# Kernel tuning notes

Measured on AMD Instinct MI355X. Metric: run time of the kernel, lower is better.

## Reference

```python
import jax, jax.numpy as jnp
import numpy as np

N_ATOMS = 2048
REPLICATES = 3          # fixed in source
CENTER_CELL = 13        # index of (0,0,0) offset among the 27 images


def setup_inputs() -> dict:
    key = jax.random.key(0)
    k1, k2, k3 = jax.random.split(key, 3)
    # Slightly perturbed cubic lattice, ~30 Angstrom box
    cell = 30.0 * jnp.eye(3, dtype=jnp.float32) + 0.5 * jax.random.normal(k1, (3, 3), dtype=jnp.float32)
    frac = jax.random.uniform(k2, (N_ATOMS, 3), dtype=jnp.float32)
    positions = frac @ cell  # cartesian positions inside the cell
    numbers = jax.random.randint(k3, (N_ATOMS,), 0, 100, dtype=jnp.int64)
    return {"positions": positions, "cell": cell, "numbers": numbers, "k": 12}


def reference(positions, cell, numbers, k):
    N = positions.shape[0]
    dt = positions.dtype
    # --- create_labeled_supercell: 3x3x3 images, offsets in {-1,0,1} ---
    r = jnp.arange(-1, 2)
    offs = jnp.stack(jnp.meshgrid(r, r, r, indexing="ij"), axis=-1).reshape(-1, 3).astype(dt)  # [27,3]
    shift = offs @ cell                                   # [27,3] cartesian shifts
    pos_sc = (positions[None, :, :] + shift[:, None, :]).reshape(-1, 3)  # [27N,3]
    # atom_id = tile(arange(N),27) => global_idx % N ; cell_id = global_idx // N
    # --- box_filter: keep points within central cell expanded by dx ---
    row_norm = jnp.linalg.norm(cell, axis=1)              # [3]
    dx = 0.1 * jnp.min(row_norm)
    frac = pos_sc @ jnp.linalg.inv(cell)                  # fractional coords [27N,3]
    eps = dx / row_norm                                   # margin in fractional units
    valid = jnp.all((frac >= -eps) & (frac <= 1.0 + eps), axis=1)  # [27N]
    # --- KNN for central-cell nodes (== periodic-graph dst nodes) ---
    center = pos_sc[CENTER_CELL * N:(CENTER_CELL + 1) * N]  # [N,3] == positions
    d2 = (jnp.sum(center * center, axis=1)[:, None]
          + jnp.sum(pos_sc * pos_sc, axis=1)[None, :]
          - 2.0 * center @ pos_sc.T)                      # [N, 27N]
    big = jnp.asarray(1e30, dt)
    d2 = jnp.where(valid[None, :], d2, big)               # drop box-filtered nodes
    self_idx = CENTER_CELL * N + jnp.arange(N)
    d2 = d2.at[jnp.arange(N), self_idx].set(big)          # exclude self-loops
    neg_d2, idx = jax.lax.top_k(-d2, k)                   # [N,k] nearest neighbors
    src_pos = pos_sc[idx]                                 # [N,k,3]
    edge_vec = (src_pos - center[:, None, :]).reshape(-1, 3)   # [N*k,3]
    dist = jnp.sqrt(jnp.maximum(-neg_d2, 0.0)).reshape(-1)     # [N*k]
    # --- create_periodic_graph: map src supercell node -> original atom_id ---
    src_atom = (idx % N).reshape(-1)                      # [N*k] int
    dst_atom = jnp.repeat(jnp.arange(N), k)               # [N*k] int
    return edge_vec, dist, src_atom, dst_atom, numbers
```

## Files before the change

### kernel.cpp

```cpp
#include <hip/hip_runtime.h>
#include <stdint.h>

#define N_ATOMS 2048
#define KNN     12
#define CAP     128
#define NEDGE   (N_ATOMS * KNN)
#define OFF_EDGE 0
#define OFF_DIST (3 * NEDGE)
#define OFF_SRC  (OFF_DIST + NEDGE)
#define OFF_DST  (OFF_SRC + NEDGE)
#define OFF_NUM  (OFF_DST + NEDGE)
#define DELTA   5e-4f

__global__ __launch_bounds__(256) void knn_fused(
    const float* __restrict__ pos, const float* __restrict__ cell,
    const int* __restrict__ numbers, float* __restrict__ out)
{
    __shared__ float sh_shift[27][3];
    __shared__ unsigned long long sh_keys[CAP];
    __shared__ int sh_cnt;

    const int a = blockIdx.x;
    const int tid = threadIdx.x;

    float c[9];
#pragma unroll
    for (int q = 0; q < 9; ++q) c[q] = cell[q];

    double a00 = c[0], a01 = c[1], a02 = c[2];
    double a10 = c[3], a11 = c[4], a12 = c[5];
    double a20 = c[6], a21 = c[7], a22 = c[8];
    double det = a00 * (a11 * a22 - a12 * a21)
               - a01 * (a10 * a22 - a12 * a20)
               + a02 * (a10 * a21 - a11 * a20);
    double id = 1.0 / det;
    float M[9];
    M[0] = (float)(( a11 * a22 - a12 * a21) * id);
    M[1] = (float)((-(a01 * a22 - a02 * a21)) * id);
    M[2] = (float)(( a01 * a12 - a02 * a11) * id);
    M[3] = (float)((-(a10 * a22 - a12 * a20)) * id);
    M[4] = (float)(( a00 * a22 - a02 * a20) * id);
    M[5] = (float)((-(a00 * a12 - a02 * a10)) * id);
    M[6] = (float)(( a10 * a21 - a11 * a20) * id);
    M[7] = (float)((-(a00 * a21 - a01 * a20)) * id);
    M[8] = (float)(( a00 * a11 - a01 * a10) * id);

    float rn0 = sqrtf(c[0]*c[0] + c[1]*c[1] + c[2]*c[2]);
    float rn1 = sqrtf(c[3]*c[3] + c[4]*c[4] + c[5]*c[5]);
    float rn2 = sqrtf(c[6]*c[6] + c[7]*c[7] + c[8]*c[8]);
    float dxm = 0.1f * fminf(rn0, fminf(rn1, rn2));
    const float e0 = dxm / rn0, e1 = dxm / rn1, e2 = dxm / rn2;

    float vol = (float)fabs(det);
    float T = powf(3.0f * 48.0f * vol / (4.0f * 3.14159265f * (float)N_ATOMS), 2.0f / 3.0f);

    if (tid < 27) {
        int j = tid;
        float o0 = (float)(j / 9 - 1);
        float o1 = (float)((j / 3) % 3 - 1);
        float o2 = (float)(j % 3 - 1);
        sh_shift[j][0] = __fadd_rn(__fadd_rn(__fmul_rn(o0, c[0]), __fmul_rn(o1, c[3])), __fmul_rn(o2, c[6]));
        sh_shift[j][1] = __fadd_rn(__fadd_rn(__fmul_rn(o0, c[1]), __fmul_rn(o1, c[4])), __fmul_rn(o2, c[7]));
        sh_shift[j][2] = __fadd_rn(__fadd_rn(__fmul_rn(o0, c[2]), __fmul_rn(o1, c[5])), __fmul_rn(o2, c[8]));
    }

    if (a < N_ATOMS / 256) {
        int mm = a * 256 + tid;
        out[OFF_NUM + mm] = (float)numbers[mm];
    }

    const float cx = pos[a * 3 + 0];
    const float cy = pos[a * 3 + 1];
    const float cz = pos[a * 3 + 2];
    const float cc = __fadd_rn(__fadd_rn(__fmul_rn(cx, cx), __fmul_rn(cy, cy)), __fmul_rn(cz, cz));

    int cnt = 0;
    for (int att = 0; att < 16; ++att) {
        if (tid == 0) sh_cnt = 0;
        __syncthreads();

#pragma unroll
        for (int ch = 0; ch < N_ATOMS / 256; ++ch) {
            int i = ch * 256 + tid;
            float pxi = pos[i * 3 + 0], pyi = pos[i * 3 + 1], pzi = pos[i * 3 + 2];
            float fr0 = __fmaf_rn(pzi, M[6], __fmaf_rn(pyi, M[3], __fmul_rn(pxi, M[0])));
            float fr1 = __fmaf_rn(pzi, M[7], __fmaf_rn(pyi, M[4], __fmul_rn(pxi, M[1])));
            float fr2 = __fmaf_rn(pzi, M[8], __fmaf_rn(pyi, M[5], __fmul_rn(pxi, M[2])));
            int alt0 = 1, has0 = 0, unc0 = 0;
            if (fr0 <= e0 + DELTA)              { alt0 = 2; has0 = 1; unc0 = (fr0 > e0 - DELTA); }
            else if (fr0 >= 1.0f - e0 - DELTA)  { alt0 = 0; has0 = 1; unc0 = (fr0 < 1.0f - e0 + DELTA); }
            int alt1 = 1, has1 = 0, unc1 = 0;
            if (fr1 <= e1 + DELTA)              { alt1 = 2; has1 = 1; unc1 = (fr1 > e1 - DELTA); }
            else if (fr1 >= 1.0f - e1 - DELTA)  { alt1 = 0; has1 = 1; unc1 = (fr1 < 1.0f - e1 + DELTA); }
            int alt2 = 1, has2 = 0, unc2 = 0;
            if (fr2 <= e2 + DELTA)              { alt2 = 2; has2 = 1; unc2 = (fr2 > e2 - DELTA); }
            else if (fr2 >= 1.0f - e2 - DELTA)  { alt2 = 0; has2 = 1; unc2 = (fr2 < 1.0f - e2 + DELTA); }

#pragma unroll
            for (int s = 0; s < 8; ++s) {
                int s0 = s & 1, s1 = (s >> 1) & 1, s2 = (s >> 2) & 1;
                if ((s0 & (has0 ^ 1)) | (s1 & (has1 ^ 1)) | (s2 & (has2 ^ 1))) continue;
                int k0 = s0 ? alt0 : 1;
                int k1 = s1 ? alt1 : 1;
                int k2 = s2 ? alt2 : 1;
                int j = k0 * 9 + k1 * 3 + k2;
                float px = __fadd_rn(pxi, sh_shift[j][0]);
                float py = __fadd_rn(pyi, sh_shift[j][1]);
                float pz = __fadd_rn(pzi, sh_shift[j][2]);
                float pp  = __fadd_rn(__fadd_rn(__fmul_rn(px, px), __fmul_rn(py, py)), __fmul_rn(pz, pz));
                float dot = __fmaf_rn(cz, pz, __fmaf_rn(cy, py, __fmul_rn(cx, px)));
                float d2  = __fsub_rn(__fadd_rn(cc, pp), __fmul_rn(2.0f, dot));
                if (d2 < T) {
                    if (i == a && j == 13) continue;
                    if ((s0 & unc0) | (s1 & unc1) | (s2 & unc2)) {
                        float f0 = __fmaf_rn(pz, M[6], __fmaf_rn(py, M[3], __fmul_rn(px, M[0])));
                        float f1 = __fmaf_rn(pz, M[7], __fmaf_rn(py, M[4], __fmul_rn(px, M[1])));
                        float f2 = __fmaf_rn(pz, M[8], __fmaf_rn(py, M[5], __fmul_rn(px, M[2])));
                        bool v = (f0 >= -e0) && (f0 <= 1.0f + e0)
                              && (f1 >= -e1) && (f1 <= 1.0f + e1)
                              && (f2 >= -e2) && (f2 <= 1.0f + e2);
                        if (!v) continue;
                    }
                    int slot = atomicAdd(&sh_cnt, 1);
                    if (slot < CAP)
                        sh_keys[slot] = ((unsigned long long)__float_as_uint(d2) << 32)
                                      | (unsigned)(j * N_ATOMS + i);
                }
            }
        }
        __syncthreads();
        cnt = sh_cnt;
        __syncthreads();
        if (cnt >= KNN && cnt <= CAP) break;
        T = (cnt < KNN) ? T * 2.0f : T * 0.5f;
    }
    if (cnt > CAP) cnt = CAP;

    if (tid < 64) {
        const unsigned long long MAXK = ~0ull;
        unsigned long long k0 = (tid < cnt) ? sh_keys[tid] : MAXK;
        unsigned long long k1 = (tid + 64 < cnt) ? sh_keys[tid + 64] : MAXK;
        unsigned long long lo = (k0 < k1) ? k0 : k1;
        unsigned long long hi = (k0 < k1) ? k1 : k0;
#pragma unroll
        for (int r = 0; r < KNN; ++r) {
            unsigned long long mn = lo;
#pragma unroll
            for (int off = 32; off; off >>= 1) {
                unsigned long long o = __shfl_xor(mn, off, 64);
                mn = (o < mn) ? o : mn;
            }
            if (lo == mn) { lo = hi; hi = MAXK; }
            if (tid == r) {
                unsigned mval = (unsigned)(mn & 0xffffffffu);
                float d2 = __uint_as_float((unsigned)(mn >> 32));
                int ii = (int)(mval & (N_ATOMS - 1));
                int jj = (int)(mval >> 11);
                float px = __fadd_rn(pos[ii * 3 + 0], sh_shift[jj][0]);
                float py = __fadd_rn(pos[ii * 3 + 1], sh_shift[jj][1]);
                float pz = __fadd_rn(pos[ii * 3 + 2], sh_shift[jj][2]);
                int eo = a * KNN + r;
                out[OFF_EDGE + 3 * eo + 0] = __fsub_rn(px, cx);
                out[OFF_EDGE + 3 * eo + 1] = __fsub_rn(py, cy);
                out[OFF_EDGE + 3 * eo + 2] = __fsub_rn(pz, cz);
                out[OFF_DIST + eo] = sqrtf(fmaxf(d2, 0.0f));
                out[OFF_SRC + eo]  = (float)ii;
                out[OFF_DST + eo]  = (float)a;
            }
        }
    }
}

extern "C" void kernel_launch(void* const* d_in, const int* in_sizes, int n_in,
                              void* d_out, int out_size, void* d_ws, size_t ws_size,
                              hipStream_t stream) {
    const float* pos     = (const float*)d_in[0];
    const float* cell    = (const float*)d_in[1];
    const int*   numbers = (const int*)d_in[2];
    float*       out     = (float*)d_out;
    (void)d_ws; (void)ws_size;

    hipLaunchKernelGGL(knn_fused, dim3(N_ATOMS), dim3(256), 0, stream,
                       pos, cell, numbers, out);
}
```

Baseline: 94.92 us.

## Build compacted periodic-image candidate list in LDS once, reuse across four centers

Each block now expands all atoms plus their needed periodic images into a compacted float4 list in shared memory. It uses wave ballots and a single atomic per wave to place entries, and tags each entry with its image id and an uncertainty flag. Four center atoms per block then scan this shared list instead of recomputing fractional coordinates and shifts from global memory for each center. This removes the per-center image-generation work and global loads. In exchange the block uses about 76KB of LDS, which lowers occupancy, and there are only 512 blocks, each processing four centers one after another.

New measurement: 102.9 us. +8.4%, slower.

```diff
diff --git a/kernel.cpp b/kernel.cpp
--- a/kernel.cpp
+++ b/kernel.cpp
@@ -4,6 +4,9 @@
 #define N_ATOMS 2048
 #define KNN     12
 #define CAP     128
+#define QCAP    4736
+#define CPB     4
+#define NBLK    (N_ATOMS / CPB)
 #define NEDGE   (N_ATOMS * KNN)
 #define OFF_EDGE 0
 #define OFF_DIST (3 * NEDGE)
@@ -16,12 +19,13 @@
     const float* __restrict__ pos, const float* __restrict__ cell,
     const int* __restrict__ numbers, float* __restrict__ out)
 {
+    __shared__ float4 sh_rec[QCAP];
     __shared__ float sh_shift[27][3];
     __shared__ unsigned long long sh_keys[CAP];
-    __shared__ int sh_cnt;
-
-    const int a = blockIdx.x;
+    __shared__ int sh_qn, sh_cnt;
+
     const int tid = threadIdx.x;
+    const int lane = tid & 63;
 
     float c[9];
 #pragma unroll
@@ -52,7 +56,7 @@
     const float e0 = dxm / rn0, e1 = dxm / rn1, e2 = dxm / rn2;
 
     float vol = (float)fabs(det);
-    float T = powf(3.0f * 48.0f * vol / (4.0f * 3.14159265f * (float)N_ATOMS), 2.0f / 3.0f);
+    const float T0 = powf(3.0f * 48.0f * vol / (4.0f * 3.14159265f * (float)N_ATOMS), 2.0f / 3.0f);
 
     if (tid < 27) {
         int j = tid;
@@ -63,26 +67,25 @@
         sh_shift[j][1] = __fadd_rn(__fadd_rn(__fmul_rn(o0, c[1]), __fmul_rn(o1, c[4])), __fmul_rn(o2, c[7]));
         sh_shift[j][2] = __fadd_rn(__fadd_rn(__fmul_rn(o0, c[2]), __fmul_rn(o1, c[5])), __fmul_rn(o2, c[8]));
     }
-
-    if (a < N_ATOMS / 256) {
-        int mm = a * 256 + tid;
+    if (tid == 0) sh_qn = N_ATOMS;
+    if (blockIdx.x < N_ATOMS / 256) {
+        int mm = blockIdx.x * 256 + tid;
         out[OFF_NUM + mm] = (float)numbers[mm];
     }
-
-    const float cx = pos[a * 3 + 0];
-    const float cy = pos[a * 3 + 1];
-    const float cz = pos[a * 3 + 2];
-    const float cc = __fadd_rn(__fadd_rn(__fmul_rn(cx, cx), __fmul_rn(cy, cy)), __fmul_rn(cz, cz));
-
-    int cnt = 0;
-    for (int att = 0; att < 16; ++att) {
-        if (tid == 0) sh_cnt = 0;
-        __syncthreads();
-
-#pragma unroll
-        for (int ch = 0; ch < N_ATOMS / 256; ++ch) {
-            int i = ch * 256 + tid;
-            float pxi = pos[i * 3 + 0], pyi = pos[i * 3 + 1], pzi = pos[i * 3 + 2];
+    __syncthreads();
+
+    {
+        const float4* pv = reinterpret_cast<const float4*>(pos + tid * 24);
+        float4 w0 = pv[0], w1 = pv[1], w2 = pv[2], w3 = pv[3], w4 = pv[4], w5 = pv[5];
+        float ax[8] = {w0.x, w0.w, w1.z, w2.y, w3.x, w3.w, w4.z, w5.y};
+        float ay[8] = {w0.y, w1.x, w1.w, w2.z, w3.y, w4.x, w4.w, w5.z};
+        float az[8] = {w0.z, w1.y, w2.x, w2.w, w3.z, w4.y, w5.x, w5.w};
+        const unsigned long long lmask_lt = (1ull << lane) - 1ull;
+
+#pragma unroll
+        for (int q = 0; q < 8; ++q) {
+            const int i = tid * 8 + q;
+            const float pxi = ax[q], pyi = ay[q], pzi = az[q];
             float fr0 = __fmaf_rn(pzi, M[6], __fmaf_rn(pyi, M[3], __fmul_rn(pxi, M[0])));
             float fr1 = __fmaf_rn(pzi, M[7], __fmaf_rn(pyi, M[4], __fmul_rn(pxi, M[1])));
             float fr2 = __fmaf_rn(pzi, M[8], __fmaf_rn(pyi, M[5], __fmul_rn(pxi, M[2])));
@@ -96,26 +99,83 @@
             if (fr2 <= e2 + DELTA)              { alt2 = 2; has2 = 1; unc2 = (fr2 > e2 - DELTA); }
             else if (fr2 >= 1.0f - e2 - DELTA)  { alt2 = 0; has2 = 1; unc2 = (fr2 < 1.0f - e2 + DELTA); }
 
-#pragma unroll
-            for (int s = 0; s < 8; ++s) {
-                int s0 = s & 1, s1 = (s >> 1) & 1, s2 = (s >> 2) & 1;
-                if ((s0 & (has0 ^ 1)) | (s1 & (has1 ^ 1)) | (s2 & (has2 ^ 1))) continue;
-                int k0 = s0 ? alt0 : 1;
-                int k1 = s1 ? alt1 : 1;
-                int k2 = s2 ? alt2 : 1;
-                int j = k0 * 9 + k1 * 3 + k2;
-                float px = __fadd_rn(pxi, sh_shift[j][0]);
-                float py = __fadd_rn(pyi, sh_shift[j][1]);
-                float pz = __fadd_rn(pzi, sh_shift[j][2]);
-                float pp  = __fadd_rn(__fadd_rn(__fmul_rn(px, px), __fmul_rn(py, py)), __fmul_rn(pz, pz));
-                float dot = __fmaf_rn(cz, pz, __fmaf_rn(cy, py, __fmul_rn(cx, px)));
-                float d2  = __fsub_rn(__fadd_rn(cc, pp), __fmul_rn(2.0f, dot));
+            {
+                float px = __fadd_rn(pxi, sh_shift[13][0]);
+                float py = __fadd_rn(pyi, sh_shift[13][1]);
+                float pz = __fadd_rn(pzi, sh_shift[13][2]);
+                sh_rec[i] = make_float4(px, py, pz,
+                    __uint_as_float((unsigned)(i | (13 << 11))));
+            }
+
+            unsigned en = 0;
+#pragma unroll
+            for (int s = 1; s < 8; ++s) {
+                bool ok = ((s & 1) ? has0 : 1) && ((s & 2) ? has1 : 1) && ((s & 4) ? has2 : 1);
+                en |= ok ? (1u << s) : 0u;
+            }
+            unsigned long long B[8];
+            int pc[8];
+            int tot = 0;
+#pragma unroll
+            for (int s = 1; s < 8; ++s) {
+                B[s] = __ballot((en >> s) & 1u);
+                pc[s] = __popcll(B[s]);
+                tot += pc[s];
+            }
+            int base = 0;
+            if (lane == 0 && tot) base = atomicAdd(&sh_qn, tot);
+            base = __shfl(base, 0, 64);
+            int run = base;
+#pragma unroll
+            for (int s = 1; s < 8; ++s) {
+                if ((en >> s) & 1u) {
+                    int slot = run + __popcll(B[s] & lmask_lt);
+                    if (slot < QCAP) {
+                        int k0 = (s & 1) ? alt0 : 1;
+                        int k1 = (s & 2) ? alt1 : 1;
+                        int k2 = (s & 4) ? alt2 : 1;
+                        int j = k0 * 9 + k1 * 3 + k2;
+                        int u = ((s & 1) & unc0) | (((s >> 1) & 1) & unc1) | (((s >> 2) & 1) & unc2);
+                        float px = __fadd_rn(pxi, sh_shift[j][0]);
+                        float py = __fadd_rn(pyi, sh_shift[j][1]);
+                        float pz = __fadd_rn(pzi, sh_shift[j][2]);
+                        sh_rec[slot] = make_float4(px, py, pz,
+                            __uint_as_float((unsigned)(i | (j << 11) | (u << 16))));
+                    }
+                }
+                run += pc[s];
+            }
+        }
+    }
+    __syncthreads();
+    const int qn = min(sh_qn, QCAP);
+
+    for (int ci = 0; ci < CPB; ++ci) {
+        const int a = blockIdx.x * CPB + ci;
+        const float cx = pos[a * 3 + 0];
+        const float cy = pos[a * 3 + 1];
+        const float cz = pos[a * 3 + 2];
+        const float ccv = __fadd_rn(__fadd_rn(__fmul_rn(cx, cx), __fmul_rn(cy, cy)), __fmul_rn(cz, cz));
+        float T = T0;
+        int cnt = 0;
+
+        for (int att = 0; att < 16; ++att) {
+            if (tid == 0) sh_cnt = 0;
+            __syncthreads();
+            for (int it = tid; it < qn; it += 256) {
+                float4 rec = sh_rec[it];
+                float pp  = __fadd_rn(__fadd_rn(__fmul_rn(rec.x, rec.x), __fmul_rn(rec.y, rec.y)), __fmul_rn(rec.z, rec.z));
+                float dot = __fmaf_rn(cz, rec.z, __fmaf_rn(cy, rec.y, __fmul_rn(cx, rec.x)));
+                float d2  = __fsub_rn(__fadd_rn(ccv, pp), __fmul_rn(2.0f, dot));
                 if (d2 < T) {
+                    unsigned meta = __float_as_uint(rec.w);
+                    int i = (int)(meta & 2047u);
+                    int j = (int)((meta >> 11) & 31u);
                     if (i == a && j == 13) continue;
-                    if ((s0 & unc0) | (s1 & unc1) | (s2 & unc2)) {
-                        float f0 = __fmaf_rn(pz, M[6], __fmaf_rn(py, M[3], __fmul_rn(px, M[0])));
-                        float f1 = __fmaf_rn(pz, M[7], __fmaf_rn(py, M[4], __fmul_rn(px, M[1])));
-                        float f2 = __fmaf_rn(pz, M[8], __fmaf_rn(py, M[5], __fmul_rn(px, M[2])));
+                    if (meta >> 16) {
+                        float f0 = __fmaf_rn(rec.z, M[6], __fmaf_rn(rec.y, M[3], __fmul_rn(rec.x, M[0])));
+                        float f1 = __fmaf_rn(rec.z, M[7], __fmaf_rn(rec.y, M[4], __fmul_rn(rec.x, M[1])));
+                        float f2 = __fmaf_rn(rec.z, M[8], __fmaf_rn(rec.y, M[5], __fmul_rn(rec.x, M[2])));
                         bool v = (f0 >= -e0) && (f0 <= 1.0f + e0)
                               && (f1 >= -e1) && (f1 <= 1.0f + e1)
                               && (f2 >= -e2) && (f2 <= 1.0f + e2);
@@ -127,47 +187,48 @@
                                       | (unsigned)(j * N_ATOMS + i);
                 }
             }
+            __syncthreads();
+            cnt = sh_cnt;
+            __syncthreads();
+            if (cnt >= KNN && cnt <= CAP) break;
+            T = (cnt < KNN) ? T * 2.0f : T * 0.5f;
+        }
+        if (cnt > CAP) cnt = CAP;
+
+        if (tid < 64) {
+            const unsigned long long MAXK = ~0ull;
+            unsigned long long k0 = (tid < cnt) ? sh_keys[tid] : MAXK;
+            unsigned long long k1 = (tid + 64 < cnt) ? sh_keys[tid + 64] : MAXK;
+            unsigned long long lo = (k0 < k1) ? k0 : k1;
+            unsigned long long hi = (k0 < k1) ? k1 : k0;
+#pragma unroll
+            for (int r = 0; r < KNN; ++r) {
+                unsigned long long mn = lo;
+#pragma unroll
+                for (int off = 32; off; off >>= 1) {
+                    unsigned long long o = __shfl_xor(mn, off, 64);
+                    mn = (o < mn) ? o : mn;
+                }
+                if (lo == mn) { lo = hi; hi = MAXK; }
+                if (tid == r) {
+                    unsigned mval = (unsigned)(mn & 0xffffffffu);
+                    float d2 = __uint_as_float((unsigned)(mn >> 32));
+                    int ii = (int)(mval & (N_ATOMS - 1));
+                    int jj = (int)(mval >> 11);
+                    float px = __fadd_rn(pos[ii * 3 + 0], sh_shift[jj][0]);
+                    float py = __fadd_rn(pos[ii * 3 + 1], sh_shift[jj][1]);
+                    float pz = __fadd_rn(pos[ii * 3 + 2], sh_shift[jj][2]);
+                    int eo = a * KNN + r;
+                    out[OFF_EDGE + 3 * eo + 0] = __fsub_rn(px, cx);
+                    out[OFF_EDGE + 3 * eo + 1] = __fsub_rn(py, cy);
+                    out[OFF_EDGE + 3 * eo + 2] = __fsub_rn(pz, cz);
+                    out[OFF_DIST + eo] = sqrtf(fmaxf(d2, 0.0f));
+                    out[OFF_SRC + eo]  = (float)ii;
+                    out[OFF_DST + eo]  = (float)a;
+                }
+            }
         }
         __syncthreads();
-        cnt = sh_cnt;
-        __syncthreads();
-        if (cnt >= KNN && cnt <= CAP) break;
-        T = (cnt < KNN) ? T * 2.0f : T * 0.5f;
-    }
-    if (cnt > CAP) cnt = CAP;
-
-    if (tid < 64) {
-        const unsigned long long MAXK = ~0ull;
-        unsigned long long k0 = (tid < cnt) ? sh_keys[tid] : MAXK;
-        unsigned long long k1 = (tid + 64 < cnt) ? sh_keys[tid + 64] : MAXK;
-        unsigned long long lo = (k0 < k1) ? k0 : k1;
-        unsigned long long hi = (k0 < k1) ? k1 : k0;
-#pragma unroll
-        for (int r = 0; r < KNN; ++r) {
-            unsigned long long mn = lo;
-#pragma unroll
-            for (int off = 32; off; off >>= 1) {
-                unsigned long long o = __shfl_xor(mn, off, 64);
-                mn = (o < mn) ? o : mn;
-            }
-            if (lo == mn) { lo = hi; hi = MAXK; }
-            if (tid == r) {
-                unsigned mval = (unsigned)(mn & 0xffffffffu);
-                float d2 = __uint_as_float((unsigned)(mn >> 32));
-                int ii = (int)(mval & (N_ATOMS - 1));
-                int jj = (int)(mval >> 11);
-                float px = __fadd_rn(pos[ii * 3 + 0], sh_shift[jj][0]);
-                float py = __fadd_rn(pos[ii * 3 + 1], sh_shift[jj][1]);
-                float pz = __fadd_rn(pos[ii * 3 + 2], sh_shift[jj][2]);
-                int eo = a * KNN + r;
-                out[OFF_EDGE + 3 * eo + 0] = __fsub_rn(px, cx);
-                out[OFF_EDGE + 3 * eo + 1] = __fsub_rn(py, cy);
-                out[OFF_EDGE + 3 * eo + 2] = __fsub_rn(pz, cz);
-                out[OFF_DIST + eo] = sqrtf(fmaxf(d2, 0.0f));
-                out[OFF_SRC + eo]  = (float)ii;
-                out[OFF_DST + eo]  = (float)a;
-            }
-        }
     }
 }
 
@@ -180,6 +241,6 @@
     float*       out     = (float*)d_out;
     (void)d_ws; (void)ws_size;
 
-    hipLaunchKernelGGL(knn_fused, dim3(N_ATOMS), dim3(256), 0, stream,
+    hipLaunchKernelGGL(knn_fused, dim3(NBLK), dim3(256), 0, stream,
                        pos, cell, numbers, out);
 }
```
